# Kernel tuning notes

Hardware: AMD Instinct MI355X
Metric: run time of the kernel (lower is better)

Reference implementation:

```python
import jax, jax.numpy as jnp
import numpy as np

H = 8
D_MODEL = 512
NEG = -1e9  # fp32 masking value from the torch source


def setup_inputs() -> dict:
    key = jax.random.key(0)
    ks = jax.random.split(key, 13)
    B, T, C, D = 2, 512, 8, D_MODEL
    s = 1.0 / np.sqrt(D)
    inp = {
        "query": jax.random.normal(ks[0], (B, T, C, D), jnp.float32),
        "key": jax.random.normal(ks[1], (B, T, C, D), jnp.float32),
        "value": jax.random.normal(ks[2], (B, T, C, D), jnp.float32),
        "mask": jax.random.randint(ks[3], (B, T, T, 1), 0, 2, jnp.int32),
        # four Linear(d_model, d_model) layers, stored as (in, out)
        "Wq": jax.random.normal(ks[4], (D, D), jnp.float32) * s,
        "bq": jax.random.normal(ks[5], (D,), jnp.float32) * s,
        "Wk": jax.random.normal(ks[6], (D, D), jnp.float32) * s,
        "bk": jax.random.normal(ks[7], (D,), jnp.float32) * s,
        "Wv": jax.random.normal(ks[8], (D, D), jnp.float32) * s,
        "bv": jax.random.normal(ks[9], (D,), jnp.float32) * s,
        "Wo": jax.random.normal(ks[10], (D, D), jnp.float32) * s,
        "bo": jax.random.normal(ks[11], (D,), jnp.float32) * s,
    }
    return inp


def _mha(query, key, value, mask, Wq, bq, Wk, bk, Wv, bv, Wo, bo):
    B, T, C, D = query.shape
    h, dk = H, D // H

    def proj(x, W, b):
        y = (x @ W + b).reshape(B, T, C, h, dk)
        return jnp.transpose(y, (0, 3, 2, 1, 4))  # [B,h,C,T,dk] (torch transpose(1,3))

    q = proj(query, Wq, bq)
    k = proj(key, Wk, bk)
    v = proj(value, Wv, bv)

    scores = jnp.einsum("bhctd,bhcsd->bhcts", q, k) / np.sqrt(dk)  # [B,h,C,T,T]
    # The torch view/transpose/view dance is just a permutation putting C last;
    # it is equivalent to masking scores[b,h,c,t,s] where mask[b,t,s,0]==0
    # (mask broadcast over heads h and channels c).
    m = mask[:, :, :, 0]  # [B,T,Tk]
    scores = jnp.where(m[:, None, None, :, :] == 0, NEG, scores)
    p_attn = jax.nn.softmax(scores, axis=-1)
    # dropout omitted (inference/deterministic reference)
    x = jnp.einsum("bhcts,bhcsd->bhctd", p_attn, v)  # [B,h,C,T,dk]
    x = jnp.transpose(x, (0, 3, 2, 1, 4)).reshape(B, T, C, D)
    return x @ Wo + bo


def reference(query, key, value, mask, Wq, bq, Wk, bk, Wv, bv, Wo, bo):
    return _mha(query, key, value, mask, Wq, bq, Wk, bk, Wv, bv, Wo, bo)
```

## Files before the change

### kernel.cpp

```cpp
#include <hip/hip_runtime.h>
#include <hip/hip_bf16.h>

typedef __bf16 bf16;
typedef __bf16 bf16x8 __attribute__((ext_vector_type(8)));
typedef float floatx4 __attribute__((ext_vector_type(4)));


#define AS1 __attribute__((address_space(1)))
#define AS3 __attribute__((address_space(3)))

__device__ __forceinline__ void gload_lds16(const bf16* g, bf16* l) {
    __builtin_amdgcn_global_load_lds((const AS1 unsigned int*)g,
                                     (AS3 unsigned int*)l, 16, 0, 0);
}

union Pack8 { bf16 h[8]; uint4 u; };

__global__ __launch_bounds__(256) void wtr_kernel(
    const float* __restrict__ Wq, const float* __restrict__ Wk,
    const float* __restrict__ Wv, const float* __restrict__ Wo,
    bf16* __restrict__ WT)
{
    __shared__ float Ts[64][65];
    const int tid = threadIdx.x;
    const int k0 = blockIdx.x * 64;
    const int n0 = blockIdx.y * 64;
    const int z  = blockIdx.z;
    const float* W = (z == 0) ? Wq : (z == 1) ? Wk : (z == 2) ? Wv : Wo;
    bf16* O = WT + (size_t)z * 512 * 512;
    #pragma unroll
    for (int i = 0; i < 16; i++) {
        const int r = i * 4 + (tid >> 6), c = tid & 63;
        Ts[r][c] = W[(size_t)(k0 + r) * 512 + n0 + c];
    }
    __syncthreads();
    #pragma unroll
    for (int i = 0; i < 16; i++) {
        const int a = i * 4 + (tid >> 6), c = tid & 63;
        O[(size_t)(n0 + a) * 512 + k0 + c] = (bf16)Ts[c][a];
    }
}

__global__ __launch_bounds__(256) void gemm_qkv(
    const float* __restrict__ Aq, const float* __restrict__ Ak,
    const float* __restrict__ Av, const bf16* __restrict__ WT,
    const float* __restrict__ Bq, const float* __restrict__ Bk,
    const float* __restrict__ Bv,
    bf16* __restrict__ Oq, bf16* __restrict__ Ok, bf16* __restrict__ Ov)
{
    __shared__ bf16 Asm[128 * 32];
    __shared__ bf16 Bsm[128 * 32];
    const int z = blockIdx.z;
    const float* A    = (z == 0) ? Aq : (z == 1) ? Ak : Av;
    const float* bias = (z == 0) ? Bq : (z == 1) ? Bk : Bv;
    bf16* out         = (z == 0) ? Oq : (z == 1) ? Ok : Ov;
    const bf16* BT = WT + (size_t)z * 262144;
    const float scale = (z == 0) ? 0.125f : 1.0f;

    const int tid  = threadIdx.x;
    const int lane = tid & 63;
    const int wave = tid >> 6;
    const int quad = lane >> 4;
    const int l16  = lane & 15;
    const int mblk = blockIdx.x * 128;
    const int nblk = blockIdx.y * 128;

    const int srow = wave * 16 + (lane >> 2);
    const int scol = (lane & 3) * 8;
    const float* Ag0 = A + (size_t)(mblk + srow) * 512 + scol;
    const float* Ag1 = Ag0 + (size_t)64 * 512;
    const bf16* Bg0 = BT + (size_t)(nblk + srow) * 512 + scol;
    const bf16* Bg1 = Bg0 + (size_t)64 * 512;
    bf16* Alp0 = Asm + srow * 32 + scol;
    bf16* Alp1 = Alp0 + 64 * 32;
    bf16* Bl0 = Bsm + wave * 16 * 32;
    bf16* Bl1 = Bsm + (64 + wave * 16) * 32;

    const int wr = (wave >> 1) * 64;
    const int wc = (wave & 1) * 64;

    floatx4 acc[4][4] = {};
    for (int k0 = 0; k0 < 512; k0 += 32) {
        gload_lds16(Bg0 + k0, Bl0);
        gload_lds16(Bg1 + k0, Bl1);
        float4 x0 = *(const float4*)(Ag0 + k0);
        float4 x1 = *(const float4*)(Ag0 + k0 + 4);
        float4 y0 = *(const float4*)(Ag1 + k0);
        float4 y1 = *(const float4*)(Ag1 + k0 + 4);
        Pack8 pa, pb;
        pa.h[0] = (bf16)x0.x; pa.h[1] = (bf16)x0.y;
        pa.h[2] = (bf16)x0.z; pa.h[3] = (bf16)x0.w;
        pa.h[4] = (bf16)x1.x; pa.h[5] = (bf16)x1.y;
        pa.h[6] = (bf16)x1.z; pa.h[7] = (bf16)x1.w;
        pb.h[0] = (bf16)y0.x; pb.h[1] = (bf16)y0.y;
        pb.h[2] = (bf16)y0.z; pb.h[3] = (bf16)y0.w;
        pb.h[4] = (bf16)y1.x; pb.h[5] = (bf16)y1.y;
        pb.h[6] = (bf16)y1.z; pb.h[7] = (bf16)y1.w;
        *(uint4*)Alp0 = pa.u;
        *(uint4*)Alp1 = pb.u;
        __syncthreads();
        bf16x8 a[4], b[4];
        #pragma unroll
        for (int mt = 0; mt < 4; mt++)
            a[mt] = *(const bf16x8*)(Asm + (wr + mt * 16 + l16) * 32 + quad * 8);
        #pragma unroll
        for (int nt = 0; nt < 4; nt++)
            b[nt] = *(const bf16x8*)(Bsm + (wc + nt * 16 + l16) * 32 + quad * 8);
        #pragma unroll
        for (int mt = 0; mt < 4; mt++)
            #pragma unroll
            for (int nt = 0; nt < 4; nt++)
                acc[mt][nt] = __builtin_amdgcn_mfma_f32_16x16x32_bf16(
                    a[mt], b[nt], acc[mt][nt], 0, 0, 0);
        __syncthreads();
    }

    #pragma unroll
    for (int mt = 0; mt < 4; mt++) {
        #pragma unroll
        for (int nt = 0; nt < 4; nt++) {
            const int colg = nblk + wc + nt * 16 + l16;
            const float bb = bias[colg];
            #pragma unroll
            for (int r = 0; r < 4; r++) {
                const int rowg = mblk + wr + mt * 16 + quad * 4 + r;
                const float v = (acc[mt][nt][r] + bb) * scale;
                const int b_ = rowg >> 12;
                const int t = (rowg >> 3) & 511;
                const int c = rowg & 7;
                const int h = colg >> 6;
                const int d = colg & 63;
                const int hd = b_ * 64 + h * 8 + c;
                const size_t addr = (z == 2)
                    ? ((size_t)hd * 64 + d) * 512 + t
                    : ((size_t)hd * 512 + t) * 64 + d;
                out[addr] = (bf16)v;
            }
        }
    }
}

template<int LAYOUT, typename TO>
__global__ __launch_bounds__(256) void gemm_bt(
    const bf16* __restrict__ A, const bf16* __restrict__ BT,
    const float* __restrict__ bias, TO* __restrict__ out)
{
    __shared__ bf16 Asm[128 * 32];
    __shared__ bf16 Bsm[128 * 32];
    const int tid  = threadIdx.x;
    const int lane = tid & 63;
    const int wave = tid >> 6;
    const int quad = lane >> 4;
    const int l16  = lane & 15;
    const int mblk = blockIdx.x * 128;
    const int nblk = blockIdx.y * 128;

    const int srow = wave * 16 + (lane >> 2);
    const int scol = (lane & 3) * 8;
    const bf16* Ag0 = A + (size_t)(mblk + srow) * 512 + scol;
    const bf16* Ag1 = Ag0 + (size_t)64 * 512;
    const bf16* Bg0 = BT + (size_t)(nblk + srow) * 512 + scol;
    const bf16* Bg1 = Bg0 + (size_t)64 * 512;
    bf16* Al0 = Asm + wave * 16 * 32;
    bf16* Al1 = Asm + (64 + wave * 16) * 32;
    bf16* Bl0 = Bsm + wave * 16 * 32;
    bf16* Bl1 = Bsm + (64 + wave * 16) * 32;

    const int wr = (wave >> 1) * 64;
    const int wc = (wave & 1) * 64;

    floatx4 acc[4][4] = {};
    for (int k0 = 0; k0 < 512; k0 += 32) {
        gload_lds16(Ag0 + k0, Al0);
        gload_lds16(Ag1 + k0, Al1);
        gload_lds16(Bg0 + k0, Bl0);
        gload_lds16(Bg1 + k0, Bl1);
        __syncthreads();
        bf16x8 a[4], b[4];
        #pragma unroll
        for (int mt = 0; mt < 4; mt++)
            a[mt] = *(const bf16x8*)(Asm + (wr + mt * 16 + l16) * 32 + quad * 8);
        #pragma unroll
        for (int nt = 0; nt < 4; nt++)
            b[nt] = *(const bf16x8*)(Bsm + (wc + nt * 16 + l16) * 32 + quad * 8);
        #pragma unroll
        for (int mt = 0; mt < 4; mt++)
            #pragma unroll
            for (int nt = 0; nt < 4; nt++)
                acc[mt][nt] = __builtin_amdgcn_mfma_f32_16x16x32_bf16(
                    a[mt], b[nt], acc[mt][nt], 0, 0, 0);
        __syncthreads();
    }

    #pragma unroll
    for (int mt = 0; mt < 4; mt++) {
        #pragma unroll
        for (int nt = 0; nt < 4; nt++) {
            const int colg = nblk + wc + nt * 16 + l16;
            const float bb = bias[colg];
            #pragma unroll
            for (int r = 0; r < 4; r++) {
                const int rowg = mblk + wr + mt * 16 + quad * 4 + r;
                const float v = acc[mt][nt][r] + bb;
                if (LAYOUT == 2) {
                    out[(size_t)rowg * 512 + colg] = (TO)v;
                } else {
                    const int b_ = rowg >> 12;
                    const int t = (rowg >> 3) & 511;
                    const int c = rowg & 7;
                    const int h = colg >> 6;
                    const int d = colg & 63;
                    const int hd = b_ * 64 + h * 8 + c;
                    const size_t addr = (LAYOUT == 0)
                        ? ((size_t)hd * 512 + t) * 64 + d
                        : ((size_t)hd * 64 + d) * 512 + t;
                    out[addr] = (TO)v;
                }
            }
        }
    }
}

#define PST 520

__global__ __launch_bounds__(256, 8) void attn_kernel(
    const bf16* __restrict__ Qws, const bf16* __restrict__ Kws,
    const bf16* __restrict__ Vtws, const int* __restrict__ mask,
    bf16* __restrict__ Xws)
{
    __shared__ bf16 MPsm[16][PST];
    __shared__ float redM[4][16];
    __shared__ float redS[4][16];
    const int tid  = threadIdx.x;
    const int wave = tid >> 6;
    const int lane = tid & 63;
    const int quad = lane >> 4;
    const int l16  = lane & 15;
    const int s_ = blockIdx.x;
    const int o_ = ((s_ & 7) << 9) | (s_ >> 3);
    const int qt = o_ & 31;
    const int hd = o_ >> 5;
    const int q0 = qt * 16;
    const int b = hd >> 6;
    const int h = (hd >> 3) & 7;
    const int c = hd & 7;

    {
        const int* mp = mask + ((size_t)b * 512 + q0) * 512;
        #pragma unroll
        for (int it = 0; it < 8; it++) {
            const int idx = (it * 256 + tid) * 4;
            const int4 mv = *(const int4*)(mp + idx);
            const int row = idx >> 9, col = idx & 511;
            union { bf16 h[4]; unsigned long long u; } pk;
            pk.h[0] = (mv.x == 0) ? (bf16)(-1.0e9f) : (bf16)0.0f;
            pk.h[1] = (mv.y == 0) ? (bf16)(-1.0e9f) : (bf16)0.0f;
            pk.h[2] = (mv.z == 0) ? (bf16)(-1.0e9f) : (bf16)0.0f;
            pk.h[3] = (mv.w == 0) ? (bf16)(-1.0e9f) : (bf16)0.0f;
            *(unsigned long long*)&MPsm[row][col] = pk.u;
        }
    }

    const bf16* Qh = Qws + (size_t)hd * 512 * 64;
    const bf16* Kh = Kws + (size_t)hd * 512 * 64;
    bf16x8 aq0 = *(const bf16x8*)(Qh + (size_t)(q0 + l16) * 64 + quad * 8);
    bf16x8 aq1 = *(const bf16x8*)(Qh + (size_t)(q0 + l16) * 64 + 32 + quad * 8);
    __syncthreads();

    float sv[8][4];
    float mx[4] = {-3.0e38f, -3.0e38f, -3.0e38f, -3.0e38f};
    #pragma unroll
    for (int nt = 0; nt < 8; nt++) {
        const int s0 = wave * 128 + nt * 16;
        bf16x8 bk0 = *(const bf16x8*)(Kh + (size_t)(s0 + l16) * 64 + quad * 8);
        bf16x8 bk1 = *(const bf16x8*)(Kh + (size_t)(s0 + l16) * 64 + 32 + quad * 8);
        floatx4 s = {};
        s = __builtin_amdgcn_mfma_f32_16x16x32_bf16(aq0, bk0, s, 0, 0, 0);
        s = __builtin_amdgcn_mfma_f32_16x16x32_bf16(aq1, bk1, s, 0, 0, 0);
        #pragma unroll
        for (int r = 0; r < 4; r++) {
            const float v = s[r] + (float)MPsm[quad * 4 + r][s0 + l16];
            sv[nt][r] = v;
            mx[r] = fmaxf(mx[r], v);
        }
    }
    #pragma unroll
    for (int off = 1; off < 16; off <<= 1)
        #pragma unroll
        for (int r = 0; r < 4; r++)
            mx[r] = fmaxf(mx[r], __shfl_xor(mx[r], off, 64));
    if (l16 == 0)
        #pragma unroll
        for (int r = 0; r < 4; r++) redM[wave][quad * 4 + r] = mx[r];
    __syncthreads();
    float mf[4], sum[4] = {0.f, 0.f, 0.f, 0.f};
    #pragma unroll
    for (int r = 0; r < 4; r++) {
        const int qr = quad * 4 + r;
        mf[r] = fmaxf(fmaxf(redM[0][qr], redM[1][qr]),
                      fmaxf(redM[2][qr], redM[3][qr]));
    }
    #pragma unroll
    for (int nt = 0; nt < 8; nt++)
        #pragma unroll
        for (int r = 0; r < 4; r++) {
            const float e = __expf(sv[nt][r] - mf[r]);
            sv[nt][r] = e;
            sum[r] += e;
        }
    #pragma unroll
    for (int off = 1; off < 16; off <<= 1)
        #pragma unroll
        for (int r = 0; r < 4; r++)
            sum[r] += __shfl_xor(sum[r], off, 64);
    if (l16 == 0)
        #pragma unroll
        for (int r = 0; r < 4; r++) redS[wave][quad * 4 + r] = sum[r];
    __syncthreads();
    float inv[4];
    #pragma unroll
    for (int r = 0; r < 4; r++) {
        const int qr = quad * 4 + r;
        inv[r] = 1.f / (redS[0][qr] + redS[1][qr] + redS[2][qr] + redS[3][qr]);
    }
    #pragma unroll
    for (int nt = 0; nt < 8; nt++)
        #pragma unroll
        for (int r = 0; r < 4; r++)
            MPsm[quad * 4 + r][wave * 128 + nt * 16 + l16] =
                (bf16)(sv[nt][r] * inv[r]);
    __syncthreads();

    const bf16* Vh = Vtws + (size_t)hd * 64 * 512;
    const int d0 = wave * 16;
    floatx4 oacc = {};
    #pragma unroll
    for (int ks = 0; ks < 16; ks++) {
        bf16x8 ap = *(const bf16x8*)(&MPsm[l16][ks * 32 + quad * 8]);
        bf16x8 bv = *(const bf16x8*)(Vh + (size_t)(d0 + l16) * 512 + ks * 32 + quad * 8);
        oacc = __builtin_amdgcn_mfma_f32_16x16x32_bf16(ap, bv, oacc, 0, 0, 0);
    }
    #pragma unroll
    for (int r = 0; r < 4; r++) {
        const int q = quad * 4 + r;
        const size_t row = ((size_t)b * 512 + q0 + q) * 8 + c;
        Xws[row * 512 + h * 64 + d0 + l16] = (bf16)oacc[r];
    }
}

extern "C" void kernel_launch(void* const* d_in, const int* in_sizes, int n_in,
                              void* d_out, int out_size, void* d_ws, size_t ws_size,
                              hipStream_t stream)
{
    const float* qin  = (const float*)d_in[0];
    const float* kin  = (const float*)d_in[1];
    const float* vin  = (const float*)d_in[2];
    const int*   mask = (const int*)d_in[3];
    const float* Bq = (const float*)d_in[5];
    const float* Bk = (const float*)d_in[7];
    const float* Bv = (const float*)d_in[9];
    const float* Bo = (const float*)d_in[11];
    float* out = (float*)d_out;

    const size_t R = (size_t)8192 * 512;
    bf16* r0 = (bf16*)d_ws;
    bf16* r1 = r0 + R;
    bf16* r2 = r1 + R;
    bf16* r3 = r2 + R;
    bf16* WT = r3 + R;

    wtr_kernel<<<dim3(8, 8, 4), dim3(256), 0, stream>>>(
        (const float*)d_in[4], (const float*)d_in[6],
        (const float*)d_in[8], (const float*)d_in[10], WT);
    gemm_qkv<<<dim3(64, 4, 3), dim3(256), 0, stream>>>(
        qin, kin, vin, WT, Bq, Bk, Bv, r0, r1, r2);
    attn_kernel<<<dim3(4096), dim3(256), 0, stream>>>(
        r0, r1, r2, mask, r3);
    gemm_bt<2, float><<<dim3(64, 4), dim3(256), 0, stream>>>(
        r3, WT + (size_t)3 * 262144, Bo, out);
}
```

Measured before the change: 232.8 us.

## Enlarge attention query tile to 64 rows and stage V-transpose writes through LDS

Each attention block now handles 64 query rows instead of 16, so every K and V tile fetched from global memory feeds four MFMA row tiles, and the grid shrinks from 4096 to 1024 blocks. The mask is read directly from global memory instead of being staged into LDS. The transposed V projection output is first written into an LDS tile and then stored to global memory as 16-byte vectorized chunks, replacing scattered 2-byte stores. In exchange, register pressure rises (32 score accumulators per lane) and launch bounds drop to 2 blocks per CU, which lowers occupancy. Uncoalesced per-element mask loads and a larger LDS footprint could offset the gain.

```diff
diff --git a/kernel.cpp b/kernel.cpp
--- a/kernel.cpp
+++ b/kernel.cpp
@@ -50,6 +50,7 @@
 {
     __shared__ bf16 Asm[128 * 32];
     __shared__ bf16 Bsm[128 * 32];
+    __shared__ bf16 Tsm[128][136];
     const int z = blockIdx.z;
     const float* A    = (z == 0) ? Aq : (z == 1) ? Ak : Av;
     const float* bias = (z == 0) ? Bq : (z == 1) ? Bk : Bv;
@@ -115,35 +116,63 @@
         __syncthreads();
     }
 
-    #pragma unroll
-    for (int mt = 0; mt < 4; mt++) {
-        #pragma unroll
-        for (int nt = 0; nt < 4; nt++) {
-            const int colg = nblk + wc + nt * 16 + l16;
-            const float bb = bias[colg];
-            #pragma unroll
-            for (int r = 0; r < 4; r++) {
-                const int rowg = mblk + wr + mt * 16 + quad * 4 + r;
-                const float v = (acc[mt][nt][r] + bb) * scale;
-                const int b_ = rowg >> 12;
-                const int t = (rowg >> 3) & 511;
-                const int c = rowg & 7;
-                const int h = colg >> 6;
-                const int d = colg & 63;
-                const int hd = b_ * 64 + h * 8 + c;
-                const size_t addr = (z == 2)
-                    ? ((size_t)hd * 64 + d) * 512 + t
-                    : ((size_t)hd * 512 + t) * 64 + d;
-                out[addr] = (bf16)v;
+    if (z != 2) {
+        #pragma unroll
+        for (int mt = 0; mt < 4; mt++) {
+            #pragma unroll
+            for (int nt = 0; nt < 4; nt++) {
+                const int colg = nblk + wc + nt * 16 + l16;
+                const float bb = bias[colg];
+                #pragma unroll
+                for (int r = 0; r < 4; r++) {
+                    const int rowg = mblk + wr + mt * 16 + quad * 4 + r;
+                    const float v = (acc[mt][nt][r] + bb) * scale;
+                    const int b_ = rowg >> 12;
+                    const int t_ = (rowg >> 3) & 511;
+                    const int c  = rowg & 7;
+                    const int h  = colg >> 6;
+                    const int d  = colg & 63;
+                    const int hd = b_ * 64 + h * 8 + c;
+                    out[((size_t)hd * 512 + t_) * 64 + d] = (bf16)v;
+                }
             }
         }
-    }
-}
-
-template<int LAYOUT, typename TO>
-__global__ __launch_bounds__(256) void gemm_bt(
+    } else {
+        #pragma unroll
+        for (int mt = 0; mt < 4; mt++) {
+            #pragma unroll
+            for (int nt = 0; nt < 4; nt++) {
+                const int cl = wc + nt * 16 + l16;
+                const float bb = bias[nblk + cl];
+                #pragma unroll
+                for (int r = 0; r < 4; r++)
+                    Tsm[wr + mt * 16 + quad * 4 + r][cl] =
+                        (bf16)(acc[mt][nt][r] + bb);
+            }
+        }
+        __syncthreads();
+        const int b_ = mblk >> 12;
+        const int t0 = (mblk >> 3) & 511;
+        #pragma unroll
+        for (int ch = tid; ch < 1024; ch += 256) {
+            const int col = ch >> 3, c = ch & 7;
+            const int h = (nblk + col) >> 6, d = (nblk + col) & 63;
+            const int hd = b_ * 64 + h * 8 + c;
+            Pack8 lo, hi;
+            #pragma unroll
+            for (int j = 0; j < 8; j++) lo.h[j] = Tsm[j * 8 + c][col];
+            #pragma unroll
+            for (int j = 0; j < 8; j++) hi.h[j] = Tsm[(j + 8) * 8 + c][col];
+            bf16* dst = out + ((size_t)hd * 64 + d) * 512 + t0;
+            *(uint4*)dst = lo.u;
+            *(uint4*)(dst + 8) = hi.u;
+        }
+    }
+}
+
+__global__ __launch_bounds__(256) void gemm_o(
     const bf16* __restrict__ A, const bf16* __restrict__ BT,
-    const float* __restrict__ bias, TO* __restrict__ out)
+    const float* __restrict__ bias, float* __restrict__ out)
 {
     __shared__ bf16 Asm[128 * 32];
     __shared__ bf16 Bsm[128 * 32];
@@ -201,21 +230,7 @@
             #pragma unroll
             for (int r = 0; r < 4; r++) {
                 const int rowg = mblk + wr + mt * 16 + quad * 4 + r;
-                const float v = acc[mt][nt][r] + bb;
-                if (LAYOUT == 2) {
-                    out[(size_t)rowg * 512 + colg] = (TO)v;
-                } else {
-                    const int b_ = rowg >> 12;
-                    const int t = (rowg >> 3) & 511;
-                    const int c = rowg & 7;
-                    const int h = colg >> 6;
-                    const int d = colg & 63;
-                    const int hd = b_ * 64 + h * 8 + c;
-                    const size_t addr = (LAYOUT == 0)
-                        ? ((size_t)hd * 512 + t) * 64 + d
-                        : ((size_t)hd * 64 + d) * 512 + t;
-                    out[addr] = (TO)v;
-                }
+                out[(size_t)rowg * 512 + colg] = acc[mt][nt][r] + bb;
             }
         }
     }
@@ -223,129 +238,162 @@
 
 #define PST 520
 
-__global__ __launch_bounds__(256, 8) void attn_kernel(
+__global__ __launch_bounds__(256, 2) void attn_kernel(
     const bf16* __restrict__ Qws, const bf16* __restrict__ Kws,
     const bf16* __restrict__ Vtws, const int* __restrict__ mask,
     bf16* __restrict__ Xws)
 {
-    __shared__ bf16 MPsm[16][PST];
-    __shared__ float redM[4][16];
-    __shared__ float redS[4][16];
+    __shared__ bf16 Psm[64][PST];
+    __shared__ float redM[4][64];
+    __shared__ float redS[4][64];
     const int tid  = threadIdx.x;
     const int wave = tid >> 6;
     const int lane = tid & 63;
     const int quad = lane >> 4;
     const int l16  = lane & 15;
     const int s_ = blockIdx.x;
-    const int o_ = ((s_ & 7) << 9) | (s_ >> 3);
-    const int qt = o_ & 31;
-    const int hd = o_ >> 5;
-    const int q0 = qt * 16;
+    const int o_ = ((s_ & 7) << 7) | (s_ >> 3);
+    const int hd = o_ >> 3;
+    const int qt = o_ & 7;
+    const int q0 = qt * 64;
     const int b = hd >> 6;
     const int h = (hd >> 3) & 7;
     const int c = hd & 7;
 
-    {
-        const int* mp = mask + ((size_t)b * 512 + q0) * 512;
-        #pragma unroll
-        for (int it = 0; it < 8; it++) {
-            const int idx = (it * 256 + tid) * 4;
-            const int4 mv = *(const int4*)(mp + idx);
-            const int row = idx >> 9, col = idx & 511;
-            union { bf16 h[4]; unsigned long long u; } pk;
-            pk.h[0] = (mv.x == 0) ? (bf16)(-1.0e9f) : (bf16)0.0f;
-            pk.h[1] = (mv.y == 0) ? (bf16)(-1.0e9f) : (bf16)0.0f;
-            pk.h[2] = (mv.z == 0) ? (bf16)(-1.0e9f) : (bf16)0.0f;
-            pk.h[3] = (mv.w == 0) ? (bf16)(-1.0e9f) : (bf16)0.0f;
-            *(unsigned long long*)&MPsm[row][col] = pk.u;
-        }
-    }
-
     const bf16* Qh = Qws + (size_t)hd * 512 * 64;
     const bf16* Kh = Kws + (size_t)hd * 512 * 64;
-    bf16x8 aq0 = *(const bf16x8*)(Qh + (size_t)(q0 + l16) * 64 + quad * 8);
-    bf16x8 aq1 = *(const bf16x8*)(Qh + (size_t)(q0 + l16) * 64 + 32 + quad * 8);
-    __syncthreads();
-
-    float sv[8][4];
-    float mx[4] = {-3.0e38f, -3.0e38f, -3.0e38f, -3.0e38f};
+    const int* mp = mask + ((size_t)b * 512 + q0) * 512;
+
+    bf16x8 aq[4][2];
+    #pragma unroll
+    for (int s = 0; s < 4; s++) {
+        aq[s][0] = *(const bf16x8*)(Qh + (size_t)(q0 + s * 16 + l16) * 64 + quad * 8);
+        aq[s][1] = *(const bf16x8*)(Qh + (size_t)(q0 + s * 16 + l16) * 64 + 32 + quad * 8);
+    }
+
+    floatx4 sv[4][8];
+    #pragma unroll
+    for (int s = 0; s < 4; s++)
+        #pragma unroll
+        for (int nt = 0; nt < 8; nt++)
+            sv[s][nt] = (floatx4){0.f, 0.f, 0.f, 0.f};
+
     #pragma unroll
     for (int nt = 0; nt < 8; nt++) {
         const int s0 = wave * 128 + nt * 16;
         bf16x8 bk0 = *(const bf16x8*)(Kh + (size_t)(s0 + l16) * 64 + quad * 8);
         bf16x8 bk1 = *(const bf16x8*)(Kh + (size_t)(s0 + l16) * 64 + 32 + quad * 8);
-        floatx4 s = {};
-        s = __builtin_amdgcn_mfma_f32_16x16x32_bf16(aq0, bk0, s, 0, 0, 0);
-        s = __builtin_amdgcn_mfma_f32_16x16x32_bf16(aq1, bk1, s, 0, 0, 0);
+        #pragma unroll
+        for (int s = 0; s < 4; s++) {
+            sv[s][nt] = __builtin_amdgcn_mfma_f32_16x16x32_bf16(
+                aq[s][0], bk0, sv[s][nt], 0, 0, 0);
+            sv[s][nt] = __builtin_amdgcn_mfma_f32_16x16x32_bf16(
+                aq[s][1], bk1, sv[s][nt], 0, 0, 0);
+        }
+    }
+
+    float mx[4][4];
+    #pragma unroll
+    for (int s = 0; s < 4; s++)
+        #pragma unroll
+        for (int r = 0; r < 4; r++)
+            mx[s][r] = -3.0e38f;
+    #pragma unroll
+    for (int s = 0; s < 4; s++)
+        #pragma unroll
+        for (int nt = 0; nt < 8; nt++)
+            #pragma unroll
+            for (int r = 0; r < 4; r++) {
+                const int mv = mp[(size_t)(s * 16 + quad * 4 + r) * 512 +
+                                  wave * 128 + nt * 16 + l16];
+                const float v = sv[s][nt][r] + ((mv == 0) ? -1.0e9f : 0.0f);
+                sv[s][nt][r] = v;
+                mx[s][r] = fmaxf(mx[s][r], v);
+            }
+    #pragma unroll
+    for (int off = 1; off < 16; off <<= 1)
+        #pragma unroll
+        for (int s = 0; s < 4; s++)
+            #pragma unroll
+            for (int r = 0; r < 4; r++)
+                mx[s][r] = fmaxf(mx[s][r], __shfl_xor(mx[s][r], off, 64));
+    if (l16 == 0)
+        #pragma unroll
+        for (int s = 0; s < 4; s++)
+            #pragma unroll
+            for (int r = 0; r < 4; r++)
+                redM[wave][s * 16 + quad * 4 + r] = mx[s][r];
+    __syncthreads();
+
+    float mf[4][4], sum[4][4];
+    #pragma unroll
+    for (int s = 0; s < 4; s++)
         #pragma unroll
         for (int r = 0; r < 4; r++) {
-            const float v = s[r] + (float)MPsm[quad * 4 + r][s0 + l16];
-            sv[nt][r] = v;
-            mx[r] = fmaxf(mx[r], v);
-        }
-    }
+            const int qr = s * 16 + quad * 4 + r;
+            mf[s][r] = fmaxf(fmaxf(redM[0][qr], redM[1][qr]),
+                             fmaxf(redM[2][qr], redM[3][qr]));
+            sum[s][r] = 0.f;
+        }
+    #pragma unroll
+    for (int s = 0; s < 4; s++)
+        #pragma unroll
+        for (int nt = 0; nt < 8; nt++)
+            #pragma unroll
+            for (int r = 0; r < 4; r++) {
+                const float e = __expf(sv[s][nt][r] - mf[s][r]);
+                sv[s][nt][r] = e;
+                sum[s][r] += e;
+            }
     #pragma unroll
     for (int off = 1; off < 16; off <<= 1)
         #pragma unroll
-        for (int r = 0; r < 4; r++)
-            mx[r] = fmaxf(mx[r], __shfl_xor(mx[r], off, 64));
+        for (int s = 0; s < 4; s++)
+            #pragma unroll
+            for (int r = 0; r < 4; r++)
+                sum[s][r] += __shfl_xor(sum[s][r], off, 64);
     if (l16 == 0)
         #pragma unroll
-        for (int r = 0; r < 4; r++) redM[wave][quad * 4 + r] = mx[r];
+        for (int s = 0; s < 4; s++)
+            #pragma unroll
+            for (int r = 0; r < 4; r++)
+                redS[wave][s * 16 + quad * 4 + r] = sum[s][r];
     __syncthreads();
-    float mf[4], sum[4] = {0.f, 0.f, 0.f, 0.f};
-    #pragma unroll
-    for (int r = 0; r < 4; r++) {
-        const int qr = quad * 4 + r;
-        mf[r] = fmaxf(fmaxf(redM[0][qr], redM[1][qr]),
-                      fmaxf(redM[2][qr], redM[3][qr]));
-    }
-    #pragma unroll
-    for (int nt = 0; nt < 8; nt++)
+
+    #pragma unroll
+    for (int s = 0; s < 4; s++)
         #pragma unroll
         for (int r = 0; r < 4; r++) {
-            const float e = __expf(sv[nt][r] - mf[r]);
-            sv[nt][r] = e;
-            sum[r] += e;
-        }
-    #pragma unroll
-    for (int off = 1; off < 16; off <<= 1)
-        #pragma unroll
-        for (int r = 0; r < 4; r++)
-            sum[r] += __shfl_xor(sum[r], off, 64);
-    if (l16 == 0)
-        #pragma unroll
-        for (int r = 0; r < 4; r++) redS[wave][quad * 4 + r] = sum[r];
-    __syncthreads();
-    float inv[4];
-    #pragma unroll
-    for (int r = 0; r < 4; r++) {
-        const int qr = quad * 4 + r;
-        inv[r] = 1.f / (redS[0][qr] + redS[1][qr] + redS[2][qr] + redS[3][qr]);
-    }
-    #pragma unroll
-    for (int nt = 0; nt < 8; nt++)
-        #pragma unroll
-        for (int r = 0; r < 4; r++)
-            MPsm[quad * 4 + r][wave * 128 + nt * 16 + l16] =
-                (bf16)(sv[nt][r] * inv[r]);
+            const int qr = s * 16 + quad * 4 + r;
+            const float inv = 1.f / (redS[0][qr] + redS[1][qr] +
+                                     redS[2][qr] + redS[3][qr]);
+            #pragma unroll
+            for (int nt = 0; nt < 8; nt++)
+                Psm[qr][wave * 128 + nt * 16 + l16] =
+                    (bf16)(sv[s][nt][r] * inv);
+        }
     __syncthreads();
 
     const bf16* Vh = Vtws + (size_t)hd * 64 * 512;
     const int d0 = wave * 16;
-    floatx4 oacc = {};
+    floatx4 o[4] = {};
     #pragma unroll
     for (int ks = 0; ks < 16; ks++) {
-        bf16x8 ap = *(const bf16x8*)(&MPsm[l16][ks * 32 + quad * 8]);
         bf16x8 bv = *(const bf16x8*)(Vh + (size_t)(d0 + l16) * 512 + ks * 32 + quad * 8);
-        oacc = __builtin_amdgcn_mfma_f32_16x16x32_bf16(ap, bv, oacc, 0, 0, 0);
-    }
-    #pragma unroll
-    for (int r = 0; r < 4; r++) {
-        const int q = quad * 4 + r;
-        const size_t row = ((size_t)b * 512 + q0 + q) * 8 + c;
-        Xws[row * 512 + h * 64 + d0 + l16] = (bf16)oacc[r];
-    }
+        #pragma unroll
+        for (int rt = 0; rt < 4; rt++) {
+            bf16x8 ap = *(const bf16x8*)(&Psm[rt * 16 + l16][ks * 32 + quad * 8]);
+            o[rt] = __builtin_amdgcn_mfma_f32_16x16x32_bf16(ap, bv, o[rt], 0, 0, 0);
+        }
+    }
+    #pragma unroll
+    for (int rt = 0; rt < 4; rt++)
+        #pragma unroll
+        for (int r = 0; r < 4; r++) {
+            const int q = q0 + rt * 16 + quad * 4 + r;
+            const size_t row = ((size_t)b * 512 + q) * 8 + c;
+            Xws[row * 512 + h * 64 + d0 + l16] = (bf16)o[rt][r];
+        }
 }
 
 extern "C" void kernel_launch(void* const* d_in, const int* in_sizes, int n_in,
@@ -374,8 +422,8 @@
         (const float*)d_in[8], (const float*)d_in[10], WT);
     gemm_qkv<<<dim3(64, 4, 3), dim3(256), 0, stream>>>(
         qin, kin, vin, WT, Bq, Bk, Bv, r0, r1, r2);
-    attn_kernel<<<dim3(4096), dim3(256), 0, stream>>>(
+    attn_kernel<<<dim3(1024), dim3(256), 0, stream>>>(
         r0, r1, r2, mask, r3);
-    gemm_bt<2, float><<<dim3(64, 4), dim3(256), 0, stream>>>(
+    gemm_o<<<dim3(64, 4), dim3(256), 0, stream>>>(
         r3, WT + (size_t)3 * 262144, Bo, out);
 }
```

Measured after the change: 204.3 us. 12.2% less time.
